# Optimization experiments

Measured on AMD Instinct MI355X. Metric: run time of the kernel, lower is better.

## Reference

```python
import jax, jax.numpy as jnp
import numpy as np

T, B, N_IN, N_OUT = 100, 512, 512, 512
DT = 1e-3
I0 = 1e-3
KAPPA = (0.75 + 0.66) / 2  # (kappa_n + kappa_p)/2
UT = 25.0e-3
TAU_AMPA = 2e-3 * UT / (KAPPA * 20.0 * I0)
TAU_GABA_B = 2e-3 * UT / (KAPPA * 5.0 * I0)
TAU_SOMA = 2e-3 * UT / (KAPPA * 5.0 * I0)
TAU_AHP = 4e-3 * UT / (KAPPA * 2.0 * I0)
ISOMA_DPI_TAU = 5 * I0
SOMA_REFP = 5e-3 / DT  # 5.0
ISOMA_RESET = 1.2 * I0
VR = ISOMA_DPI_TAU + I0
ISOMA_TH = 2000 * I0
ISOMA_PFB_TH = 1000 * I0
ALPHA_SOMA = 4.0
AMPA_GAIN = 4 * 100 * I0
GABA_B_GAIN = 4 * 100 * I0
AHP_GAIN = 4 * 2 * I0
AHP_JUMP = 4 * I0
ISOMA_PFB_NORM = 20 * I0
ISOMA_PFB_GAIN = 100 * I0


def ste_round(x):
    # straight-through round (Round.apply): round fwd, identity bwd
    return x + jax.lax.stop_gradient(jnp.round(x) - x)


@jax.custom_vjp
def spike(x):
    # fast_sigmoid surrogate spike: heaviside fwd, 1/(10|x|+1)^2 surrogate bwd
    return (x > 0).astype(x.dtype)


def _spike_fwd(x):
    return spike(x), x


def _spike_bwd(x, g):
    return (g / (10.0 * jnp.abs(x) + 1.0) ** 2,)


spike.defvjp(_spike_fwd, _spike_bwd)


def _run(input_ampa, input_gaba_b, weight_ampa, weight_gaba_b):
    batch = input_ampa.shape[1]
    sg = jax.lax.stop_gradient
    wa = ste_round(weight_ampa)
    wg = ste_round(weight_gaba_b)
    dtype = input_ampa.dtype
    init = (
        jnp.full((batch, N_OUT), 1.1 * I0, dtype),   # Isoma_mem
        jnp.full((batch, N_OUT), I0, dtype),          # Iampa
        jnp.full((batch, N_OUT), I0, dtype),          # Igaba_b
        jnp.zeros((batch, N_OUT), dtype),             # Isoma_ahp
        jnp.zeros((batch, N_OUT), dtype),             # refractory
    )

    def step(state, inp):
        Isoma_mem, Iampa, Igaba_b, Isoma_ahp, refractory = state
        xa, xg = inp
        Isoma_pfb = sg(ISOMA_PFB_GAIN / (1.0 + jnp.exp(-(Isoma_mem - ISOMA_PFB_TH) / ISOMA_PFB_NORM)))
        Isoma_ahp_d = sg(Isoma_ahp)
        dAHP = (-AHP_GAIN - Isoma_ahp_d) / (TAU_AHP * (1.0 + AHP_GAIN / Isoma_ahp_d))
        Iin = jnp.maximum(Iampa - Igaba_b + I0, I0)
        Isoma_sum = VR + Isoma_ahp_d - Isoma_pfb
        dIsoma_mem = (ALPHA_SOMA * (Iin - Isoma_sum) - Isoma_sum * Isoma_mem / ISOMA_DPI_TAU) / (
            TAU_SOMA * (1.0 + ALPHA_SOMA * ISOMA_DPI_TAU / sg(Isoma_mem)))
        dIampa = (I0 - Iampa) / TAU_AMPA  # uses pre-injection Iampa
        Iampa = Iampa + AMPA_GAIN * (xa @ wa)
        dIgaba_b = (I0 - Igaba_b) / TAU_GABA_B
        Igaba_b = Igaba_b + GABA_B_GAIN * (xg @ wg)
        refractory = refractory - (refractory > 0).astype(dtype)
        Isoma_mem = Isoma_mem + DT * dIsoma_mem * (refractory <= 0).astype(dtype)
        Isoma_ahp = Isoma_ahp_d + DT * dAHP
        Iampa = Iampa + DT * dIampa
        Igaba_b = Igaba_b + DT * dIgaba_b
        S = spike(Isoma_mem - ISOMA_TH)
        refractory = refractory + jnp.floor(S * SOMA_REFP)  # (S*refP).long()
        Isoma_ahp = Isoma_ahp + AHP_JUMP * S
        Isoma_mem = ISOMA_RESET * S + Isoma_mem * (1.0 - S)
        Isoma_mem = jnp.maximum(Isoma_mem, I0)
        return (Isoma_mem, Iampa, Igaba_b, Isoma_ahp, refractory), S

    _, S_seq = jax.lax.scan(step, init, (input_ampa, input_gaba_b))
    return S_seq  # [T, B, N_OUT]


def setup_inputs() -> dict:
    key = jax.random.key(0)
    k1, k2, k3, k4 = jax.random.split(key, 4)
    return {
        "input_ampa": jax.random.uniform(k1, (T, B, N_IN), jnp.float32),
        "input_gaba_b": jax.random.uniform(k2, (T, B, N_IN), jnp.float32),
        "weight_ampa": jax.random.uniform(k3, (N_IN, N_OUT), jnp.float32),
        "weight_gaba_b": jax.random.uniform(k4, (N_IN, N_OUT), jnp.float32),
    }


def reference(input_ampa, input_gaba_b, weight_ampa, weight_gaba_b):
    return _run(input_ampa, input_gaba_b, weight_ampa, weight_gaba_b)
```

## Files before the change

### kernel.cpp

```cpp
#include <hip/hip_runtime.h>
#include <cmath>

namespace {
constexpr int TT = 100;
constexpr int B = 512;
constexpr int NIN = 512;
constexpr int NOUT = 512;
constexpr int NEURONS = B * NOUT;
constexpr int K3B = 3 * NIN;

constexpr double D_I0 = 1e-3;
constexpr double D_KAPPA = (0.75 + 0.66) / 2.0;
constexpr double D_UT = 25.0e-3;
constexpr float F_I0 = (float)D_I0;
constexpr float F_TAU_AMPA = (float)(2e-3 * D_UT / (D_KAPPA * 20.0 * D_I0));
constexpr float F_TAU_GABA = (float)(2e-3 * D_UT / (D_KAPPA * 5.0 * D_I0));
constexpr float F_TAU_SOMA = (float)(2e-3 * D_UT / (D_KAPPA * 5.0 * D_I0));
constexpr float F_TAU_AHP  = (float)(4e-3 * D_UT / (D_KAPPA * 2.0 * D_I0));
constexpr float F_DPI_TAU  = (float)(5.0 * D_I0);
constexpr float F_RESET    = (float)(1.2 * D_I0);
constexpr float F_VR       = (float)(5.0 * D_I0 + D_I0);
constexpr float F_TH       = (float)(2000.0 * D_I0);
constexpr float F_PFB_TH   = (float)(1000.0 * D_I0);
constexpr float F_ALPHA    = 4.0f;
constexpr float F_AMPA_GAIN = (float)(4.0 * 100.0 * D_I0);
constexpr float F_GABA_GAIN = (float)(4.0 * 100.0 * D_I0);
constexpr float F_AHP_GAIN  = (float)(4.0 * 2.0 * D_I0);
constexpr float F_AHP_JUMP  = (float)(4.0 * D_I0);
constexpr float F_PFB_NORM  = (float)(20.0 * D_I0);
constexpr float F_PFB_GAIN  = (float)(100.0 * D_I0);
constexpr float F_ALPHA_DPI = (float)(4.0 * (5.0 * D_I0));
constexpr float F_DT = 1e-3f;
constexpr float F_INIT_MEM = (float)(1.1 * D_I0);
constexpr float F_INV223 = 1.1920928955078125e-7f;
constexpr unsigned BIAS_MUL = (1u << 14) + (1u << 22);
}

typedef __attribute__((ext_vector_type(4))) int i32x4;

__device__ __forceinline__ void gload_lds16(const void* g, void* l) {
  __builtin_amdgcn_global_load_lds(
      (const __attribute__((address_space(1))) void*)g,
      (__attribute__((address_space(3))) void*)l, 16, 0, 0);
}

__global__ __launch_bounds__(256) void build_wt(
    const float* __restrict__ Wa, const float* __restrict__ Wg,
    unsigned char* __restrict__ WTa, unsigned char* __restrict__ WTg) {
  const int t = blockIdx.x * 256 + threadIdx.x;
  const float* W = (t >> 15) ? Wg : Wa;
  unsigned char* O = (t >> 15) ? WTg : WTa;
  const int r = t & 32767;
  const int n = r >> 6, k8 = r & 63;
  unsigned char b[8];
#pragma unroll
  for (int j = 0; j < 8; ++j)
    b[j] = (unsigned char)(int)rintf(W[(size_t)(k8 * 8 + j) * 512 + n]);
  const size_t addr = (size_t)(n >> 7) * 65536 + (k8 >> 3) * 8192 +
                      ((n >> 4) & 7) * 1024 +
                      ((k8 & 7) >> 1) * 256 + (n & 15) * 16 + (k8 & 1) * 8;
  *(unsigned long long*)(O + addr) = *(unsigned long long*)b;
}

__global__ __launch_bounds__(256) void colsum_w(
    const float* __restrict__ Wa, const float* __restrict__ Wg,
    int* __restrict__ colsum) {
  const int t = blockIdx.x * 256 + threadIdx.x;
  const int z = t >> 9, n = t & 511;
  const float* W = z ? Wg : Wa;
  int s = 0;
  for (int k = 0; k < 512; ++k) s += (int)rintf(W[(size_t)k * 512 + n]);
  colsum[t] = s;
}

__global__ __launch_bounds__(256) void split3(
    const float* __restrict__ XA, const float* __restrict__ XG,
    unsigned char* __restrict__ A4a, unsigned char* __restrict__ A4g, int nwpi) {
  const int wid = (blockIdx.x * 256 + threadIdx.x) >> 6;
  const int l = threadIdx.x & 63;
  const float* X = XA;
  unsigned char* O = A4a;
  int w = wid;
  if (w >= nwpi) { X = XG; O = A4g; w -= nwpi; }
  const int rt = w >> 6, rem = w & 63, c = rem >> 3, g = rem & 7;
  const int rl = l >> 2, q = l & 3;
  const float* src = X + (size_t)(rt * 128 + g * 16 + rl) * 512 + c * 64 + q * 16;
  float a[16];
#pragma unroll
  for (int j = 0; j < 4; ++j) {
    const float4 v = *(const float4*)(src + j * 4);
    a[j * 4 + 0] = v.x; a[j * 4 + 1] = v.y; a[j * 4 + 2] = v.z; a[j * 4 + 3] = v.w;
  }
  unsigned int k[16];
#pragma unroll
  for (int e = 0; e < 16; ++e) k[e] = (unsigned int)rintf(a[e] * 8388608.0f);
  unsigned char* base = O + (size_t)rt * 196608 + c * 8192 + g * 1024 + q * 256 + rl * 16;
  unsigned int u[4];
#pragma unroll
  for (int j = 0; j < 4; ++j)
    u[j] = (k[4 * j] & 127u) | ((k[4 * j + 1] & 127u) << 8) |
           ((k[4 * j + 2] & 127u) << 16) | ((k[4 * j + 3] & 127u) << 24);
  *(uint4*)(base) = make_uint4(u[0], u[1], u[2], u[3]);
#pragma unroll
  for (int j = 0; j < 4; ++j)
    u[j] = (((k[4 * j] >> 7) - 128u) & 255u) | ((((k[4 * j + 1] >> 7) - 128u) & 255u) << 8) |
           ((((k[4 * j + 2] >> 7) - 128u) & 255u) << 16) | ((((k[4 * j + 3] >> 7) - 128u) & 255u) << 24);
  *(uint4*)(base + 65536) = make_uint4(u[0], u[1], u[2], u[3]);
#pragma unroll
  for (int j = 0; j < 4; ++j)
    u[j] = (((k[4 * j] >> 15) - 128u) & 255u) | ((((k[4 * j + 1] >> 15) - 128u) & 255u) << 8) |
           ((((k[4 * j + 2] >> 15) - 128u) & 255u) << 16) | ((((k[4 * j + 3] >> 15) - 128u) & 255u) << 24);
  *(uint4*)(base + 131072) = make_uint4(u[0], u[1], u[2], u[3]);
}

__global__ __launch_bounds__(256) void gemm_i8_v8(
    const unsigned char* __restrict__ A4a, const unsigned char* __restrict__ A4g,
    const unsigned char* __restrict__ WTa, const unsigned char* __restrict__ WTg,
    const int* __restrict__ colsum,
    float* __restrict__ INCa, float* __restrict__ INCg, int nwg) {
  __shared__ __align__(16) unsigned char LDS[32768];
  unsigned char* Al = LDS;
  unsigned char* Bl = LDS + 16384;
  const int bid = blockIdx.x;
  const int L = (bid & 7) * (nwg >> 3) + (bid >> 3);
  const int m = L >> 3, sub = L & 7;
  const int n = sub & 3, z = sub >> 2;
  const unsigned char* A4 = (z ? A4g : A4a) + (size_t)m * 196608;
  const unsigned char* Bg = (z ? WTg : WTa) + (size_t)n * 65536;
  float* C = z ? INCg : INCa;

  const int tid = threadIdx.x;
  const int lane = tid & 63, wave = tid >> 6;
  const int wr = wave >> 1, wc = wave & 1;
  const int fr = lane & 15, fq = lane >> 4;
  const int goff = tid * 16;
  const int woff = wave * 1024;
  const int floc = fq * 256 + fr * 16;

#pragma unroll
  for (int j = 0; j < 2; ++j) {
    gload_lds16(A4 + 131072 + j * 4096 + goff, Al + j * 4096 + woff);
    gload_lds16(Bg + j * 4096 + goff, Bl + j * 4096 + woff);
  }

  i32x4 acc[4][4] = {};
  int buf = 0;
#pragma unroll
  for (int s = 0; s < 24; ++s) {
    __syncthreads();
    if (s < 23) {
      const int s1 = s + 1;
      const int aoff = (2 - (s1 >> 3)) * 65536 + (s1 & 7) * 8192;
      const int boff = (s1 & 7) * 8192;
      const int lb = (buf ^ 1) * 8192 + woff;
#pragma unroll
      for (int j = 0; j < 2; ++j) {
        gload_lds16(A4 + aoff + j * 4096 + goff, Al + lb + j * 4096);
        gload_lds16(Bg + boff + j * 4096 + goff, Bl + lb + j * 4096);
      }
    }
    {
      i32x4 af[4], bf[4];
#pragma unroll
      for (int fm = 0; fm < 4; ++fm)
        af[fm] = *(const i32x4*)&Al[buf * 8192 + (wr * 4 + fm) * 1024 + floc];
#pragma unroll
      for (int fn = 0; fn < 4; ++fn)
        bf[fn] = *(const i32x4*)&Bl[buf * 8192 + (wc * 4 + fn) * 1024 + floc];
#pragma unroll
      for (int fm = 0; fm < 4; ++fm)
#pragma unroll
        for (int fn = 0; fn < 4; ++fn)
          acc[fm][fn] = __builtin_amdgcn_mfma_i32_16x16x64_i8(
              af[fm], bf[fn], acc[fm][fn], 0, 0, 0);
    }
    if (s == 7) {
#pragma unroll
      for (int fm = 0; fm < 4; ++fm)
#pragma unroll
        for (int fn = 0; fn < 4; ++fn) acc[fm][fn] = acc[fm][fn] << 8;
    }
    if (s == 15) {
#pragma unroll
      for (int fm = 0; fm < 4; ++fm)
#pragma unroll
        for (int fn = 0; fn < 4; ++fn) acc[fm][fn] = acc[fm][fn] << 7;
    }
    buf ^= 1;
  }
  __syncthreads();

  const int crow0 = m * 128 + wr * 64;
  const int ccol0 = n * 128 + wc * 64;
  unsigned bias[4];
#pragma unroll
  for (int fn = 0; fn < 4; ++fn)
    bias[fn] = BIAS_MUL * (unsigned)colsum[z * 512 + ccol0 + fn * 16 + fr];
  float* scratch = (float*)LDS + wave * (16 * 68);
  const int erow = lane >> 4;
  const int ecol = (lane & 15) * 4;
#pragma unroll
  for (int fm = 0; fm < 4; ++fm) {
#pragma unroll
    for (int fn = 0; fn < 4; ++fn)
#pragma unroll
      for (int r = 0; r < 4; ++r) {
        const unsigned tot = (unsigned)acc[fm][fn][r] + bias[fn];
        scratch[(fq * 4 + r) * 68 + fn * 16 + fr] = (float)tot * F_INV223;
      }
    float4 rows[4];
#pragma unroll
    for (int j = 0; j < 4; ++j)
      rows[j] = *(const float4*)&scratch[(erow + 4 * j) * 68 + ecol];
#pragma unroll
    for (int j = 0; j < 4; ++j) {
      const int grow = crow0 + fm * 16 + erow + 4 * j;
      *(float4*)&C[(size_t)grow * NOUT + ccol0 + ecol] = rows[j];
    }
  }
}

__global__ __launch_bounds__(256) void neuron_scan(
    const float* __restrict__ inca, const float* __restrict__ incg,
    float* __restrict__ Sout, float* __restrict__ state, int tc, int first) {
  const int idx = blockIdx.x * 256 + threadIdx.x;
  float mem, ampa, gaba, ahp, refr;
  if (first) {
    mem = F_INIT_MEM; ampa = F_I0; gaba = F_I0; ahp = 0.0f; refr = 0.0f;
  } else {
    mem  = state[idx];
    ampa = state[NEURONS + idx];
    gaba = state[2 * NEURONS + idx];
    ahp  = state[3 * NEURONS + idx];
    refr = state[4 * NEURONS + idx];
  }
  for (int t = 0; t < tc; ++t) {
    const float xa = F_AMPA_GAIN * inca[(size_t)t * NEURONS + idx];
    const float xg = F_GABA_GAIN * incg[(size_t)t * NEURONS + idx];
    const float pfb = F_PFB_GAIN / (1.0f + expf(-(mem - F_PFB_TH) / F_PFB_NORM));
    const float dahp = (-F_AHP_GAIN - ahp) / (F_TAU_AHP * (1.0f + F_AHP_GAIN / ahp));
    const float Iin = fmaxf(ampa - gaba + F_I0, F_I0);
    const float Isum = F_VR + ahp - pfb;
    const float dmem = (F_ALPHA * (Iin - Isum) - Isum * mem / F_DPI_TAU)
                     / (F_TAU_SOMA * (1.0f + F_ALPHA_DPI / mem));
    const float dampa = (F_I0 - ampa) / F_TAU_AMPA;
    ampa = ampa + xa;
    const float dgaba = (F_I0 - gaba) / F_TAU_GABA;
    gaba = gaba + xg;
    refr = refr - (refr > 0.0f ? 1.0f : 0.0f);
    mem = mem + F_DT * dmem * (refr <= 0.0f ? 1.0f : 0.0f);
    ahp = ahp + F_DT * dahp;
    ampa = ampa + F_DT * dampa;
    gaba = gaba + F_DT * dgaba;
    const float S = (mem - F_TH) > 0.0f ? 1.0f : 0.0f;
    refr = refr + floorf(S * 5.0f);
    ahp = ahp + F_AHP_JUMP * S;
    mem = F_RESET * S + mem * (1.0f - S);
    mem = fmaxf(mem, F_I0);
    Sout[(size_t)t * NEURONS + idx] = S;
  }
  state[idx] = mem;
  state[NEURONS + idx] = ampa;
  state[2 * NEURONS + idx] = gaba;
  state[3 * NEURONS + idx] = ahp;
  state[4 * NEURONS + idx] = refr;
}

extern "C" void kernel_launch(void* const* d_in, const int* in_sizes, int n_in,
                              void* d_out, int out_size, void* d_ws, size_t ws_size,
                              hipStream_t stream) {
  const float* XA = (const float*)d_in[0];
  const float* XG = (const float*)d_in[1];
  const float* WA = (const float*)d_in[2];
  const float* WG = (const float*)d_in[3];
  float* S = (float*)d_out;

  int tc = 1;
  const int cands[8] = {100, 50, 25, 20, 10, 5, 2, 1};
  for (int i = 0; i < 8; ++i) {
    const size_t need = 5771264ull + (size_t)cands[i] * 3670016ull;
    if (need <= ws_size) { tc = cands[i]; break; }
  }

  unsigned char* WTa = (unsigned char*)d_ws;
  unsigned char* WTg = WTa + (size_t)NOUT * 512;
  int* colsum = (int*)(WTg + (size_t)NOUT * 512);
  unsigned char* A4a = (unsigned char*)(colsum + 1024);
  unsigned char* A4g = A4a + (size_t)tc * B * K3B;
  float* INCa  = (float*)(A4g + (size_t)tc * B * K3B);
  float* INCg  = INCa + (size_t)tc * NEURONS;
  float* state = INCg + (size_t)tc * NEURONS;

  build_wt<<<256, 256, 0, stream>>>(WA, WG, WTa, WTg);
  colsum_w<<<4, 256, 0, stream>>>(WA, WG, colsum);

  const int nwpi = tc * 256;
  const int splitBlocks = nwpi / 2;
  const int nm = tc * B / 128;
  const int nwg = nm * 8;
  const int nch = TT / tc;
  for (int c = 0; c < nch; ++c) {
    const size_t inOff = (size_t)c * tc * B * NIN;
    split3<<<splitBlocks, 256, 0, stream>>>(XA + inOff, XG + inOff, A4a, A4g, nwpi);
    gemm_i8_v8<<<nwg, 256, 0, stream>>>(A4a, A4g, WTa, WTg, colsum, INCa, INCg, nwg);
    neuron_scan<<<NEURONS / 256, 256, 0, stream>>>(
        INCa, INCg, S + (size_t)c * tc * NEURONS, state, tc, c == 0 ? 1 : 0);
  }
}
```

Before: 391.5 us.

## Widen int8 GEMM tile to 128x256 and cap time-chunk size at 20

The int8 MFMA GEMM block tile grows from 128x128 to 128x256: each wave now holds 4x8 accumulator fragments, B is double-buffered in 16 KB LDS halves, and the epilogue writes rows of 128 floats. This halves how often each A tile is re-read per output column and halves the workgroup count. The time-chunk candidates now start at 20 instead of 100, so the split/gemm/scan launch sequence runs at least five times, probably to keep intermediates cache-resident. Costs include much higher register pressure from the 128 int32 accumulator vectors per lane, more LDS per block, lower occupancy, and extra launch overhead.

```diff
diff --git a/kernel.cpp b/kernel.cpp
--- a/kernel.cpp
+++ b/kernel.cpp
@@ -113,20 +113,20 @@
   *(uint4*)(base + 131072) = make_uint4(u[0], u[1], u[2], u[3]);
 }
 
-__global__ __launch_bounds__(256) void gemm_i8_v8(
+__global__ __launch_bounds__(256) void gemm_i8_v9(
     const unsigned char* __restrict__ A4a, const unsigned char* __restrict__ A4g,
     const unsigned char* __restrict__ WTa, const unsigned char* __restrict__ WTg,
     const int* __restrict__ colsum,
     float* __restrict__ INCa, float* __restrict__ INCg, int nwg) {
-  __shared__ __align__(16) unsigned char LDS[32768];
+  __shared__ __align__(16) unsigned char LDS[49152];
   unsigned char* Al = LDS;
   unsigned char* Bl = LDS + 16384;
   const int bid = blockIdx.x;
   const int L = (bid & 7) * (nwg >> 3) + (bid >> 3);
-  const int m = L >> 3, sub = L & 7;
-  const int n = sub & 3, z = sub >> 2;
+  const int m = L >> 2, sub = L & 3;
+  const int n = sub & 1, z = sub >> 1;
   const unsigned char* A4 = (z ? A4g : A4a) + (size_t)m * 196608;
-  const unsigned char* Bg = (z ? WTg : WTa) + (size_t)n * 65536;
+  const unsigned char* Bg = (z ? WTg : WTa) + (size_t)n * 131072;
   float* C = z ? INCg : INCa;
 
   const int tid = threadIdx.x;
@@ -138,12 +138,14 @@
   const int floc = fq * 256 + fr * 16;
 
 #pragma unroll
-  for (int j = 0; j < 2; ++j) {
+  for (int j = 0; j < 2; ++j)
     gload_lds16(A4 + 131072 + j * 4096 + goff, Al + j * 4096 + woff);
-    gload_lds16(Bg + j * 4096 + goff, Bl + j * 4096 + woff);
-  }
-
-  i32x4 acc[4][4] = {};
+#pragma unroll
+  for (int j = 0; j < 4; ++j)
+    gload_lds16(Bg + (j >> 1) * 65536 + (j & 1) * 4096 + goff,
+                Bl + j * 4096 + woff);
+
+  i32x4 acc[4][8] = {};
   int buf = 0;
 #pragma unroll
   for (int s = 0; s < 24; ++s) {
@@ -152,25 +154,27 @@
       const int s1 = s + 1;
       const int aoff = (2 - (s1 >> 3)) * 65536 + (s1 & 7) * 8192;
       const int boff = (s1 & 7) * 8192;
-      const int lb = (buf ^ 1) * 8192 + woff;
-#pragma unroll
-      for (int j = 0; j < 2; ++j) {
-        gload_lds16(A4 + aoff + j * 4096 + goff, Al + lb + j * 4096);
-        gload_lds16(Bg + boff + j * 4096 + goff, Bl + lb + j * 4096);
-      }
+#pragma unroll
+      for (int j = 0; j < 2; ++j)
+        gload_lds16(A4 + aoff + j * 4096 + goff,
+                    Al + (buf ^ 1) * 8192 + j * 4096 + woff);
+#pragma unroll
+      for (int j = 0; j < 4; ++j)
+        gload_lds16(Bg + (j >> 1) * 65536 + boff + (j & 1) * 4096 + goff,
+                    Bl + (buf ^ 1) * 16384 + j * 4096 + woff);
     }
     {
-      i32x4 af[4], bf[4];
+      i32x4 af[4], bf[8];
 #pragma unroll
       for (int fm = 0; fm < 4; ++fm)
         af[fm] = *(const i32x4*)&Al[buf * 8192 + (wr * 4 + fm) * 1024 + floc];
 #pragma unroll
-      for (int fn = 0; fn < 4; ++fn)
-        bf[fn] = *(const i32x4*)&Bl[buf * 8192 + (wc * 4 + fn) * 1024 + floc];
+      for (int fn = 0; fn < 8; ++fn)
+        bf[fn] = *(const i32x4*)&Bl[buf * 16384 + (wc * 8 + fn) * 1024 + floc];
 #pragma unroll
       for (int fm = 0; fm < 4; ++fm)
 #pragma unroll
-        for (int fn = 0; fn < 4; ++fn)
+        for (int fn = 0; fn < 8; ++fn)
           acc[fm][fn] = __builtin_amdgcn_mfma_i32_16x16x64_i8(
               af[fm], bf[fn], acc[fm][fn], 0, 0, 0);
     }
@@ -178,44 +182,41 @@
 #pragma unroll
       for (int fm = 0; fm < 4; ++fm)
 #pragma unroll
-        for (int fn = 0; fn < 4; ++fn) acc[fm][fn] = acc[fm][fn] << 8;
+        for (int fn = 0; fn < 8; ++fn) acc[fm][fn] = acc[fm][fn] << 8;
     }
     if (s == 15) {
 #pragma unroll
       for (int fm = 0; fm < 4; ++fm)
 #pragma unroll
-        for (int fn = 0; fn < 4; ++fn) acc[fm][fn] = acc[fm][fn] << 7;
+        for (int fn = 0; fn < 8; ++fn) acc[fm][fn] = acc[fm][fn] << 7;
     }
     buf ^= 1;
   }
   __syncthreads();
 
   const int crow0 = m * 128 + wr * 64;
-  const int ccol0 = n * 128 + wc * 64;
-  unsigned bias[4];
-#pragma unroll
-  for (int fn = 0; fn < 4; ++fn)
+  const int ccol0 = n * 256 + wc * 128;
+  unsigned bias[8];
+#pragma unroll
+  for (int fn = 0; fn < 8; ++fn)
     bias[fn] = BIAS_MUL * (unsigned)colsum[z * 512 + ccol0 + fn * 16 + fr];
-  float* scratch = (float*)LDS + wave * (16 * 68);
-  const int erow = lane >> 4;
-  const int ecol = (lane & 15) * 4;
+  float* scratch = (float*)LDS + wave * (16 * 132);
+  const int jlane = lane & 31;
+  const int jhalf = lane >> 5;
 #pragma unroll
   for (int fm = 0; fm < 4; ++fm) {
 #pragma unroll
-    for (int fn = 0; fn < 4; ++fn)
+    for (int fn = 0; fn < 8; ++fn)
 #pragma unroll
       for (int r = 0; r < 4; ++r) {
         const unsigned tot = (unsigned)acc[fm][fn][r] + bias[fn];
-        scratch[(fq * 4 + r) * 68 + fn * 16 + fr] = (float)tot * F_INV223;
+        scratch[(fq * 4 + r) * 132 + fn * 16 + fr] = (float)tot * F_INV223;
       }
-    float4 rows[4];
-#pragma unroll
-    for (int j = 0; j < 4; ++j)
-      rows[j] = *(const float4*)&scratch[(erow + 4 * j) * 68 + ecol];
-#pragma unroll
-    for (int j = 0; j < 4; ++j) {
-      const int grow = crow0 + fm * 16 + erow + 4 * j;
-      *(float4*)&C[(size_t)grow * NOUT + ccol0 + ecol] = rows[j];
+#pragma unroll
+    for (int j = 0; j < 8; ++j) {
+      const int row = j * 2 + jhalf;
+      const float4 v = *(const float4*)&scratch[row * 132 + jlane * 4];
+      *(float4*)&C[(size_t)(crow0 + fm * 16 + row) * NOUT + ccol0 + jlane * 4] = v;
     }
   }
 }
@@ -276,8 +277,8 @@
   float* S = (float*)d_out;
 
   int tc = 1;
-  const int cands[8] = {100, 50, 25, 20, 10, 5, 2, 1};
-  for (int i = 0; i < 8; ++i) {
+  const int cands[6] = {20, 10, 5, 4, 2, 1};
+  for (int i = 0; i < 6; ++i) {
     const size_t need = 5771264ull + (size_t)cands[i] * 3670016ull;
     if (need <= ws_size) { tc = cands[i]; break; }
   }
@@ -297,12 +298,12 @@
   const int nwpi = tc * 256;
   const int splitBlocks = nwpi / 2;
   const int nm = tc * B / 128;
-  const int nwg = nm * 8;
+  const int nwg = nm * 4;
   const int nch = TT / tc;
   for (int c = 0; c < nch; ++c) {
     const size_t inOff = (size_t)c * tc * B * NIN;
     split3<<<splitBlocks, 256, 0, stream>>>(XA + inOff, XG + inOff, A4a, A4g, nwpi);
-    gemm_i8_v8<<<nwg, 256, 0, stream>>>(A4a, A4g, WTa, WTg, colsum, INCa, INCg, nwg);
+    gemm_i8_v9<<<nwg, 256, 0, stream>>>(A4a, A4g, WTa, WTg, colsum, INCa, INCg, nwg);
     neuron_scan<<<NEURONS / 256, 256, 0, stream>>>(
         INCa, INCg, S + (size_t)c * tc * NEURONS, state, tc, c == 0 ? 1 : 0);
   }
```

Measured after the change: 420.6 us. 1.07x slower.

## Deepen int8 GEMM LDS pipeline to four buffers with three stages prefetched

Applied to the files above, without the earlier changes.

The GEMM main loop moves from a double-buffered LDS scheme, which prefetches one K-stage ahead, to a four-slot ring that prefetches three stages ahead. It uses explicit vmcnt waits plus a raw s_barrier, so only the oldest in-flight stage has to land before each step. The goal is to hide global-to-LDS latency behind MFMA work. In exchange, LDS use doubles to 64KB per block, which may reduce the number of resident workgroups per CU, and the hand-coded waitcnt logic is fragile.

```diff
diff --git a/kernel.cpp b/kernel.cpp
--- a/kernel.cpp
+++ b/kernel.cpp
@@ -44,6 +44,8 @@
       (__attribute__((address_space(3))) void*)l, 16, 0, 0);
 }
 
+#define WAITVM(N) asm volatile("s_waitcnt vmcnt(" #N ")" ::: "memory")
+
 __global__ __launch_bounds__(256) void build_wt(
     const float* __restrict__ Wa, const float* __restrict__ Wg,
     unsigned char* __restrict__ WTa, unsigned char* __restrict__ WTg) {
@@ -113,14 +115,14 @@
   *(uint4*)(base + 131072) = make_uint4(u[0], u[1], u[2], u[3]);
 }
 
-__global__ __launch_bounds__(256) void gemm_i8_v8(
+__global__ __launch_bounds__(256) void gemm_i8_v10(
     const unsigned char* __restrict__ A4a, const unsigned char* __restrict__ A4g,
     const unsigned char* __restrict__ WTa, const unsigned char* __restrict__ WTg,
     const int* __restrict__ colsum,
     float* __restrict__ INCa, float* __restrict__ INCg, int nwg) {
-  __shared__ __align__(16) unsigned char LDS[32768];
+  __shared__ __align__(16) unsigned char LDS[65536];
   unsigned char* Al = LDS;
-  unsigned char* Bl = LDS + 16384;
+  unsigned char* Bl = LDS + 32768;
   const int bid = blockIdx.x;
   const int L = (bid & 7) * (nwg >> 3) + (bid >> 3);
   const int m = L >> 3, sub = L & 7;
@@ -137,36 +139,38 @@
   const int woff = wave * 1024;
   const int floc = fq * 256 + fr * 16;
 
-#pragma unroll
-  for (int j = 0; j < 2; ++j) {
-    gload_lds16(A4 + 131072 + j * 4096 + goff, Al + j * 4096 + woff);
-    gload_lds16(Bg + j * 4096 + goff, Bl + j * 4096 + woff);
-  }
+#define STAGE(t)                                                            \
+  {                                                                         \
+    const int aoff_ = (2 - ((t) >> 3)) * 65536 + ((t) & 7) * 8192;          \
+    const int boff_ = ((t) & 7) * 8192;                                     \
+    const int lb_ = ((t) & 3) * 8192 + woff;                                \
+    gload_lds16(A4 + aoff_ + goff, Al + lb_);                               \
+    gload_lds16(A4 + aoff_ + 4096 + goff, Al + lb_ + 4096);                 \
+    gload_lds16(Bg + boff_ + goff, Bl + lb_);                               \
+    gload_lds16(Bg + boff_ + 4096 + goff, Bl + lb_ + 4096);                 \
+  }
+
+  STAGE(0) STAGE(1) STAGE(2)
 
   i32x4 acc[4][4] = {};
-  int buf = 0;
 #pragma unroll
   for (int s = 0; s < 24; ++s) {
-    __syncthreads();
-    if (s < 23) {
-      const int s1 = s + 1;
-      const int aoff = (2 - (s1 >> 3)) * 65536 + (s1 & 7) * 8192;
-      const int boff = (s1 & 7) * 8192;
-      const int lb = (buf ^ 1) * 8192 + woff;
-#pragma unroll
-      for (int j = 0; j < 2; ++j) {
-        gload_lds16(A4 + aoff + j * 4096 + goff, Al + lb + j * 4096);
-        gload_lds16(Bg + boff + j * 4096 + goff, Bl + lb + j * 4096);
-      }
-    }
+    if (s <= 21) WAITVM(8);
+    else if (s == 22) WAITVM(4);
+    else WAITVM(0);
+    __builtin_amdgcn_s_barrier();
+    asm volatile("" ::: "memory");
+    __builtin_amdgcn_sched_barrier(0);
+    if (s + 3 < 24) STAGE(s + 3)
     {
+      const int b = (s & 3) * 8192;
       i32x4 af[4], bf[4];
 #pragma unroll
       for (int fm = 0; fm < 4; ++fm)
-        af[fm] = *(const i32x4*)&Al[buf * 8192 + (wr * 4 + fm) * 1024 + floc];
+        af[fm] = *(const i32x4*)&Al[b + (wr * 4 + fm) * 1024 + floc];
 #pragma unroll
       for (int fn = 0; fn < 4; ++fn)
-        bf[fn] = *(const i32x4*)&Bl[buf * 8192 + (wc * 4 + fn) * 1024 + floc];
+        bf[fn] = *(const i32x4*)&Bl[b + (wc * 4 + fn) * 1024 + floc];
 #pragma unroll
       for (int fm = 0; fm < 4; ++fm)
 #pragma unroll
@@ -186,8 +190,8 @@
 #pragma unroll
         for (int fn = 0; fn < 4; ++fn) acc[fm][fn] = acc[fm][fn] << 7;
     }
-    buf ^= 1;
-  }
+  }
+#undef STAGE
   __syncthreads();
 
   const int crow0 = m * 128 + wr * 64;
@@ -302,7 +306,7 @@
   for (int c = 0; c < nch; ++c) {
     const size_t inOff = (size_t)c * tc * B * NIN;
     split3<<<splitBlocks, 256, 0, stream>>>(XA + inOff, XG + inOff, A4a, A4g, nwpi);
-    gemm_i8_v8<<<nwg, 256, 0, stream>>>(A4a, A4g, WTa, WTg, colsum, INCa, INCg, nwg);
+    gemm_i8_v10<<<nwg, 256, 0, stream>>>(A4a, A4g, WTa, WTg, colsum, INCa, INCg, nwg);
     neuron_scan<<<NEURONS / 256, 256, 0, stream>>>(
         INCa, INCg, S + (size_t)c * tc * NEURONS, state, tc, c == 0 ? 1 : 0);
   }
```

Result: faster. 348.3 us (-11.0%).
